# Optimization experiments

Hardware: AMD Instinct MI355X
Metric: run time of the kernel (lower is better)

## Reference

```python
import jax, jax.numpy as jnp
import numpy as np

B, T, H, V, ADIM, AMAX = 16, 1024, 512, 32000, 512, 10


def setup_inputs() -> dict:
    key = jax.random.key(0)
    ks = jax.random.split(key, 24)
    def n(k, shape, s=0.05):
        return jax.random.normal(k, shape, jnp.float32) * s
    return {
        "instruction": jax.random.randint(ks[0], (B, T), 0, V, dtype=jnp.int32),
        "emb": n(ks[1], (V, H)),
        "wih_f": n(ks[2], (4 * H, H)), "whh_f": n(ks[3], (4 * H, H)),
        "bih_f": n(ks[4], (4 * H,)), "bhh_f": n(ks[5], (4 * H,)),
        "wih_b": n(ks[6], (4 * H, H)), "whh_b": n(ks[7], (4 * H, H)),
        "bih_b": n(ks[8], (4 * H,)), "bhh_b": n(ks[9], (4 * H,)),
        "wg": n(ks[10], (2 * H, 2 * H)), "bg": n(ks[11], (2 * H,)),
        "ws1": n(ks[12], (H, 2 * H)), "bs1": n(ks[13], (H,)),
        "ws2": n(ks[14], (1, H)), "bs2": n(ks[15], (1,)),
        "wd1": n(ks[16], (H, 2 * H)), "bd1": n(ks[17], (H,)),
        "wd2": n(ks[18], (ADIM, H)), "bd2": n(ks[19], (ADIM,)),
        "max_actions": AMAX,
    }


def _lstm(x, wih, whh, bias):
    # x: [B, T, H] -> outputs [B, T, H]; PyTorch gate order i, f, g, o
    h0 = jnp.zeros((x.shape[0], whh.shape[1]), x.dtype)
    def step(carry, xt):
        h, c = carry
        g = xt @ wih.T + h @ whh.T + bias
        i, f, gg, o = jnp.split(g, 4, axis=-1)
        c = jax.nn.sigmoid(f) * c + jax.nn.sigmoid(i) * jnp.tanh(gg)
        h = jax.nn.sigmoid(o) * jnp.tanh(c)
        return (h, c), h
    _, hs = jax.lax.scan(step, (h0, h0), jnp.swapaxes(x, 0, 1))
    return jnp.swapaxes(hs, 0, 1)


def reference(instruction, emb, wih_f, whh_f, bih_f, bhh_f, wih_b, whh_b, bih_b, bhh_b,
              wg, bg, ws1, bs1, ws2, bs2, wd1, bd1, wd2, bd2, max_actions):
    x = emb[instruction]                                   # [B, T, H]
    fwd = _lstm(x, wih_f, whh_f, bih_f + bhh_f)            # [B, T, H]
    bwd = _lstm(x[:, ::-1], wih_b, whh_b, bih_b + bhh_b)[:, ::-1]
    enc = jnp.concatenate([fwd, bwd], axis=-1)             # [B, T, 2H]
    # sequence_lengths=None: h_n[0]=fwd last step, h_n[1]=bwd at t=0
    pooled = jnp.concatenate([fwd[:, -1], bwd[:, 0]], axis=-1)
    gctx = pooled @ wg.T + bg                               # [B, 2H]
    sh = jax.nn.relu(enc @ ws1.T + bs1)
    seg_probs = jax.nn.sigmoid((sh @ ws2.T + bs2)[..., 0])  # [B, T]
    mask = seg_probs > 0.5
    count = mask.sum(axis=-1)
    # first max_actions True positions per row (stable sort keeps time order)
    order = jnp.argsort(jnp.logical_not(mask), axis=1, stable=True)[:, :max_actions]
    gathered = jnp.take_along_axis(enc, order[..., None], axis=1)  # [B, A, 2H]
    slots = jnp.arange(max_actions)
    valid = slots[None, :] < jnp.minimum(count, max_actions)[:, None]
    empty = ((count == 0)[:, None]) & (slots[None, :] == 0)  # fallback: decode global ctx
    dec_in = jnp.where(valid[..., None], gathered, 0.0)
    dec_in = jnp.where(empty[..., None], gctx[:, None, :], dec_in)
    dh = jax.nn.relu(dec_in @ wd1.T + bd1)
    actions = (dh @ wd2.T + bd2) * (valid | empty)[..., None].astype(dec_in.dtype)
    return actions, seg_probs
```

## Files before the change

### kernel.cpp

```cpp
#include <hip/hip_runtime.h>
#include <math.h>

#define T   1024
#define NB  16
#define HD  512

#define OFF_BAR  0
#define OFF_HH   256
#define OFF_SH   (OFF_HH + 16777216)
#define OFF_SEGP (OFF_SH + 8388608)
#define OFF_GCTX (OFF_SEGP + 16384)
#define OFF_SEL  (OFF_GCTX + 16384)

typedef unsigned long long u64;

__device__ __forceinline__ float sigmoidf_(float x){ return 1.0f/(1.0f + __expf(-x)); }
__device__ __forceinline__ float tanhf_(float x){ return 1.0f - 2.0f/(1.0f + __expf(2.0f*x)); }

__global__ __launch_bounds__(512, 1)
void lstm_kernel(const int* __restrict__ instr, const float* __restrict__ emb,
                 const float* __restrict__ wih_f, const float* __restrict__ whh_f,
                 const float* __restrict__ bih_f, const float* __restrict__ bhh_f,
                 const float* __restrict__ wih_b, const float* __restrict__ whh_b,
                 const float* __restrict__ bih_b, const float* __restrict__ bhh_b,
                 float* __restrict__ ws)
{
    float* h_hist = ws + OFF_HH;

    const int wg     = blockIdx.x;
    const int dir    = wg & 1;
    const int bgrp   = (wg >> 1) & 3;
    const int uslice = wg >> 3;
    const int U      = uslice * 16;
    const int b0     = bgrp * 4;

    const float* wih = dir ? wih_b : wih_f;
    const float* whh = dir ? whh_b : whh_f;
    const float* bih = dir ? bih_b : bih_f;
    const float* bhh = dir ? bhh_b : bhh_f;

    const int tid  = threadIdx.x;
    const int wid  = tid >> 6;
    const int lane = tid & 63;
    const int rg   = wid;

    float wi[64], wh[64];
#pragma unroll
    for (int ri = 0; ri < 8; ++ri){
        int rgl = rg*8 + ri;
        int gate = rgl >> 4, ul = rgl & 15;
        size_t row = (size_t)(gate*HD + U + ul) * HD + lane*8;
        float4 a0 = *(const float4*)(wih + row);
        float4 a1 = *(const float4*)(wih + row + 4);
        float4 b0v = *(const float4*)(whh + row);
        float4 b1v = *(const float4*)(whh + row + 4);
        wi[ri*8+0]=a0.x; wi[ri*8+1]=a0.y; wi[ri*8+2]=a0.z; wi[ri*8+3]=a0.w;
        wi[ri*8+4]=a1.x; wi[ri*8+5]=a1.y; wi[ri*8+6]=a1.z; wi[ri*8+7]=a1.w;
        wh[ri*8+0]=b0v.x; wh[ri*8+1]=b0v.y; wh[ri*8+2]=b0v.z; wh[ri*8+3]=b0v.w;
        wh[ri*8+4]=b1v.x; wh[ri*8+5]=b1v.y; wh[ri*8+6]=b1v.z; wh[ri*8+7]=b1v.w;
    }

    float bI, bF, bG, bO, cst = 0.0f;
    {
        int u = tid & 15;
        bI = bih[0*HD + U + u] + bhh[0*HD + U + u];
        bF = bih[1*HD + U + u] + bhh[1*HD + U + u];
        bG = bih[2*HD + U + u] + bhh[2*HD + U + u];
        bO = bih[3*HD + U + u] + bhh[3*HD + U + u];
    }

    __shared__ float hxch[8*4*64];
    __shared__ float gbuf[256];

    const int jown = ((lane&1)<<4)|((lane&2)<<2)|(lane&4)|((lane&8)>>2)|((lane&16)>>4);
    const int own_bi  = jown >> 3;
    const int own_rgl = rg*8 + (jown & 7);
    const int gslot   = (own_rgl >> 4)*64 + own_bi*16 + (own_rgl & 15);

    for (int s = 0; s < T; ++s){
        const int tp = dir ? (T-1-s) : s;

        float a[32];
#pragma unroll
        for (int j = 0; j < 32; ++j) a[j] = 0.0f;

#pragma unroll
        for (int bi = 0; bi < 4; ++bi){
            int b = b0 + bi;
            int idx = instr[b*T + tp];
            const float* px = emb + (size_t)idx*HD + lane*8;
            float4 x0 = *(const float4*)px;
            float4 x1 = *(const float4*)(px + 4);
            float xs[8] = {x0.x,x0.y,x0.z,x0.w,x1.x,x1.y,x1.z,x1.w};
#pragma unroll
            for (int kk = 0; kk < 8; ++kk){
                float xv = xs[kk];
#pragma unroll
                for (int ri = 0; ri < 8; ++ri)
                    a[bi*8+ri] = fmaf(xv, wi[ri*8+kk], a[bi*8+ri]);
            }
        }

        if (s > 0){
            const int tprev = dir ? (T - s) : (s - 1);
            const float* hbase = h_hist + (size_t)(dir*T + tprev)*NB*HD;

            if (wid == 0){
                u64 pq[16];
                for (;;){
#pragma unroll
                    for (int bi = 0; bi < 4; ++bi){
                        const u64* p = (const u64*)(hbase + (size_t)(b0+bi)*HD + lane*8);
#pragma unroll
                        for (int q = 0; q < 4; ++q)
                            pq[bi*4+q] = __hip_atomic_load(p + q, __ATOMIC_RELAXED, __HIP_MEMORY_SCOPE_AGENT);
                    }
                    unsigned ok = 1u;
#pragma unroll
                    for (int j = 0; j < 16; ++j){
                        ok &= ((unsigned)(pq[j]      ) != 0xFFFFFFFFu) ? 1u : 0u;
                        ok &= ((unsigned)(pq[j] >> 32) != 0xFFFFFFFFu) ? 1u : 0u;
                    }
                    if (__all(ok != 0u)) break;
                    __builtin_amdgcn_s_sleep(1);
                }
#pragma unroll
                for (int bi = 0; bi < 4; ++bi){
#pragma unroll
                    for (int q = 0; q < 4; ++q){
                        hxch[(2*q  )*256 + bi*64 + lane] = __uint_as_float((unsigned)(pq[bi*4+q]      ));
                        hxch[(2*q+1)*256 + bi*64 + lane] = __uint_as_float((unsigned)(pq[bi*4+q] >> 32));
                    }
                }
            }
            __syncthreads();

#pragma unroll
            for (int bi = 0; bi < 4; ++bi){
                float hs[8];
#pragma unroll
                for (int kk = 0; kk < 8; ++kk)
                    hs[kk] = hxch[kk*256 + bi*64 + lane];
#pragma unroll
                for (int kk = 0; kk < 8; ++kk){
                    float hv = hs[kk];
#pragma unroll
                    for (int ri = 0; ri < 8; ++ri)
                        a[bi*8+ri] = fmaf(hv, wh[ri*8+kk], a[bi*8+ri]);
                }
            }
        }

#pragma unroll
        for (int m = 0; m < 5; ++m){
            const int half = 16 >> m;
            const bool up = (lane >> m) & 1;
#pragma unroll
            for (int j = 0; j < 16; ++j){
                if (j < half){
                    float lo = a[j], hi = a[j+half];
                    float rlo = __shfl_xor(lo, 1<<m, 64);
                    float rhi = __shfl_xor(hi, 1<<m, 64);
                    a[j] = up ? (hi + rhi) : (lo + rlo);
                }
            }
        }
        a[0] += __shfl_xor(a[0], 32, 64);

        if ((lane & 32) == 0) gbuf[gslot] = a[0];
        __syncthreads();

        if (tid < 64){
            float iv = sigmoidf_(gbuf[      tid] + bI);
            float fv = sigmoidf_(gbuf[ 64 + tid] + bF);
            float gv = tanhf_  (gbuf[128 + tid] + bG);
            float ov = sigmoidf_(gbuf[192 + tid] + bO);
            cst = fv*cst + iv*gv;
            float hv = ov * tanhf_(cst);
            int b = b0 + (tid >> 4), u = tid & 15;
            __hip_atomic_store(&h_hist[((size_t)(dir*T + tp)*NB + b)*HD + U + u], hv,
                               __ATOMIC_RELAXED, __HIP_MEMORY_SCOPE_AGENT);
        }
    }
}

__global__ __launch_bounds__(256, 2)
void seg_gemm(const float* __restrict__ ws_, const float* __restrict__ ws1,
              const float* __restrict__ bs1)
{
    const float* h_hist = ws_ + OFF_HH;
    float* SH = (float*)(ws_ + OFF_SH);
    __shared__ float As[64][17];
    __shared__ float Bs[64][17];
    const int m0 = blockIdx.x * 64;
    const int n0 = blockIdx.y * 64;
    const int tid = threadIdx.x;
    const int r  = tid >> 2;
    const int kq = (tid & 3) * 4;
    const int ty = tid >> 4, tx = tid & 15;
    const int bI = m0 >> 10;
    const int t0 = m0 & 1023;

    float acc[4][4];
#pragma unroll
    for (int i=0;i<4;i++)
#pragma unroll
        for (int j=0;j<4;j++) acc[i][j]=0.0f;

    for (int kb = 0; kb < 1024; kb += 16){
        int kk = kb + kq;
        const float* ap = (kk < 512)
            ? h_hist + ((size_t)(t0 + r)*NB + bI)*HD + kk
            : h_hist + ((size_t)(T + t0 + r)*NB + bI)*HD + (kk - 512);
        float4 av = *(const float4*)ap;
        As[r][kq+0]=av.x; As[r][kq+1]=av.y; As[r][kq+2]=av.z; As[r][kq+3]=av.w;
        float4 bv = *(const float4*)(ws1 + (size_t)(n0 + r)*1024 + kk);
        Bs[r][kq+0]=bv.x; Bs[r][kq+1]=bv.y; Bs[r][kq+2]=bv.z; Bs[r][kq+3]=bv.w;
        __syncthreads();
#pragma unroll
        for (int k2 = 0; k2 < 16; ++k2){
            float av_[4], bv_[4];
#pragma unroll
            for (int i=0;i<4;i++) av_[i] = As[ty*4+i][k2];
#pragma unroll
            for (int j=0;j<4;j++) bv_[j] = Bs[tx*4+j][k2];
#pragma unroll
            for (int i=0;i<4;i++)
#pragma unroll
                for (int j=0;j<4;j++) acc[i][j] = fmaf(av_[i], bv_[j], acc[i][j]);
        }
        __syncthreads();
    }
#pragma unroll
    for (int i=0;i<4;i++){
        int m = m0 + ty*4 + i;
#pragma unroll
        for (int j=0;j<4;j++){
            int n = n0 + tx*4 + j;
            SH[(size_t)m*512 + n] = fmaxf(acc[i][j] + bs1[n], 0.0f);
        }
    }
}

__global__ void seg_score(const float* __restrict__ ws_, const float* __restrict__ ws2,
                          const float* __restrict__ bs2, float* __restrict__ dout)
{
    const float* SH = ws_ + OFF_SH;
    float* segp = (float*)(ws_ + OFF_SEGP);
    int row  = blockIdx.x*4 + (threadIdx.x >> 6);
    int lane = threadIdx.x & 63;
    const float* p = SH + (size_t)row*512 + lane*8;
    const float* q = ws2 + lane*8;
    float4 a0=*(const float4*)p, a1=*(const float4*)(p+4);
    float4 b0=*(const float4*)q, b1=*(const float4*)(q+4);
    float ssum = a0.x*b0.x + a0.y*b0.y + a0.z*b0.z + a0.w*b0.w
               + a1.x*b1.x + a1.y*b1.y + a1.z*b1.z + a1.w*b1.w;
#pragma unroll
    for (int m=1;m<64;m<<=1) ssum += __shfl_xor(ssum, m, 64);
    if (lane == 0){
        float z = ssum + bs2[0];
        float pr = 1.0f/(1.0f + __expf(-z));
        segp[row] = pr;
        dout[81920 + row] = pr;
    }
}

__global__ void select_gctx(float* __restrict__ ws_, const float* __restrict__ wgm,
                            const float* __restrict__ bgv)
{
    const float* h_hist = ws_ + OFF_HH;
    const float* segp   = ws_ + OFF_SEGP;
    float* gctx = ws_ + OFF_GCTX;
    int* sel = (int*)(ws_ + OFF_SEL);
    int b = blockIdx.x, tid = threadIdx.x;
    __shared__ unsigned char flag[1024];
    __shared__ float pool[1024];
    for (int j = tid; j < 1024; j += 256){
        flag[j] = segp[b*1024 + j] > 0.5f ? 1 : 0;
        pool[j] = (j < 512) ? h_hist[((size_t)1023*NB + b)*HD + j]
                            : h_hist[((size_t)T*NB + b)*HD + (j - 512)];
    }
    __syncthreads();
    if (tid == 0){
        int c = 0;
        int tmp[10];
        for (int j = 0; j < 10; ++j) tmp[j] = 0;
        for (int t = 0; t < 1024; ++t){
            if (flag[t]){ if (c < 10) tmp[c] = t; c++; }
        }
        for (int j = 0; j < 10; ++j) sel[b*12 + j] = tmp[j];
        sel[b*12 + 10] = c;
        sel[b*12 + 11] = 0;
    }
    __syncthreads();
    for (int n = tid; n < 1024; n += 256){
        float acc = bgv[n];
        const float* wr = wgm + (size_t)n*1024;
        for (int k = 0; k < 1024; k += 4){
            acc += wr[k]*pool[k] + wr[k+1]*pool[k+1] + wr[k+2]*pool[k+2] + wr[k+3]*pool[k+3];
        }
        gctx[b*1024 + n] = acc;
    }
}

__global__ void decode(const float* __restrict__ ws_, const float* __restrict__ wd1,
                       const float* __restrict__ bd1, const float* __restrict__ wd2,
                       const float* __restrict__ bd2, float* __restrict__ dout)
{
    const float* h_hist = ws_ + OFF_HH;
    const float* gctx   = ws_ + OFF_GCTX;
    const int* sel = (const int*)(ws_ + OFF_SEL);
    int blk = blockIdx.x;
    int b = blk / 10, slot = blk % 10;
    int tid = threadIdx.x;
    int count = sel[b*12 + 10];
    int nval = count < 10 ? count : 10;
    bool empty = (count == 0);
    float* outp = dout + (size_t)(b*10 + slot)*512;
    if (slot >= nval && !(empty && slot == 0)){
        for (int n = tid; n < 512; n += 256) outp[n] = 0.0f;
        return;
    }
    __shared__ float row[1024];
    __shared__ float dh[512];
    if (empty){
        for (int j = tid; j < 1024; j += 256) row[j] = gctx[b*1024 + j];
    } else {
        int t = sel[b*12 + slot];
        for (int j = tid; j < 1024; j += 256)
            row[j] = (j < 512) ? h_hist[((size_t)t*NB + b)*HD + j]
                               : h_hist[((size_t)(T + t)*NB + b)*HD + (j-512)];
    }
    __syncthreads();
    for (int d = tid; d < 512; d += 256){
        float acc = bd1[d];
        const float* wr = wd1 + (size_t)d*1024;
        for (int k = 0; k < 1024; ++k) acc += wr[k]*row[k];
        dh[d] = fmaxf(acc, 0.0f);
    }
    __syncthreads();
    for (int n = tid; n < 512; n += 256){
        float acc = bd2[n];
        const float* wr = wd2 + (size_t)n*512;
        for (int k = 0; k < 512; ++k) acc += wr[k]*dh[k];
        outp[n] = acc;
    }
}

extern "C" void kernel_launch(void* const* d_in, const int* in_sizes, int n_in,
                              void* d_out, int out_size, void* d_ws, size_t ws_size,
                              hipStream_t stream)
{
    const int*   instr = (const int*)d_in[0];
    const float* emb   = (const float*)d_in[1];
    const float* wih_f = (const float*)d_in[2];
    const float* whh_f = (const float*)d_in[3];
    const float* bih_f = (const float*)d_in[4];
    const float* bhh_f = (const float*)d_in[5];
    const float* wih_b = (const float*)d_in[6];
    const float* whh_b = (const float*)d_in[7];
    const float* bih_b = (const float*)d_in[8];
    const float* bhh_b = (const float*)d_in[9];
    const float* wg_   = (const float*)d_in[10];
    const float* bg_   = (const float*)d_in[11];
    const float* ws1   = (const float*)d_in[12];
    const float* bs1   = (const float*)d_in[13];
    const float* ws2   = (const float*)d_in[14];
    const float* bs2   = (const float*)d_in[15];
    const float* wd1   = (const float*)d_in[16];
    const float* bd1   = (const float*)d_in[17];
    const float* wd2   = (const float*)d_in[18];
    const float* bd2   = (const float*)d_in[19];
    float* out = (float*)d_out;
    float* ws  = (float*)d_ws;

    hipMemsetAsync((char*)d_ws + (size_t)OFF_HH*4, 0xFF, (size_t)16777216*4, stream);

    hipLaunchKernelGGL(lstm_kernel, dim3(256), dim3(512), 0, stream,
                       instr, emb, wih_f, whh_f, bih_f, bhh_f,
                       wih_b, whh_b, bih_b, bhh_b, ws);
    hipLaunchKernelGGL(seg_gemm, dim3(256, 8), dim3(256), 0, stream, ws, ws1, bs1);
    hipLaunchKernelGGL(seg_score, dim3(4096), dim3(256), 0, stream, ws, ws2, bs2, out);
    hipLaunchKernelGGL(select_gctx, dim3(16), dim3(256), 0, stream, ws, wg_, bg_);
    hipLaunchKernelGGL(decode, dim3(160), dim3(256), 0, stream, ws, wd1, bd1, wd2, bd2, out);
}
```

Before: 4.390 ms.

## Poll per-group step counters before loading recurrent hidden state

Adds per-(direction, batch-group) flag arrays that each workgroup bumps after finishing a step. Waiters spin on a small 32-int flag vector instead of repeatedly atomically reloading the full hidden-state slice and checking for sentinel values. After the flags pass, the hidden state is read with plain vector loads, and the old sentinel check stays as a fallback re-read. The flag store is relaxed and not ordered after the other threads' h stores, so the sentinel check is still needed for correctness; it adds an extra flag store per step.

```diff
diff --git a/kernel.cpp b/kernel.cpp
--- a/kernel.cpp
+++ b/kernel.cpp
@@ -16,6 +16,18 @@
 
 __device__ __forceinline__ float sigmoidf_(float x){ return 1.0f/(1.0f + __expf(-x)); }
 __device__ __forceinline__ float tanhf_(float x){ return 1.0f - 2.0f/(1.0f + __expf(2.0f*x)); }
+
+__device__ __forceinline__ bool clean8(const float4* hq){
+    unsigned ok = 1u;
+#pragma unroll
+    for (int q = 0; q < 8; ++q){
+        ok &= (__float_as_uint(hq[q].x) != 0xFFFFFFFFu) ? 1u : 0u;
+        ok &= (__float_as_uint(hq[q].y) != 0xFFFFFFFFu) ? 1u : 0u;
+        ok &= (__float_as_uint(hq[q].z) != 0xFFFFFFFFu) ? 1u : 0u;
+        ok &= (__float_as_uint(hq[q].w) != 0xFFFFFFFFu) ? 1u : 0u;
+    }
+    return ok != 0u;
+}
 
 __global__ __launch_bounds__(512, 1)
 void lstm_kernel(const int* __restrict__ instr, const float* __restrict__ emb,
@@ -26,6 +38,7 @@
                  float* __restrict__ ws)
 {
     float* h_hist = ws + OFF_HH;
+    int* flags = (int*)ws;
 
     const int wg     = blockIdx.x;
     const int dir    = wg & 1;
@@ -33,6 +46,8 @@
     const int uslice = wg >> 3;
     const int U      = uslice * 16;
     const int b0     = bgrp * 4;
+
+    int* barf = flags + (dir*4 + bgrp)*32;
 
     const float* wih = dir ? wih_b : wih_f;
     const float* whh = dir ? whh_b : whh_f;
@@ -106,31 +121,46 @@
             const float* hbase = h_hist + (size_t)(dir*T + tprev)*NB*HD;
 
             if (wid == 0){
-                u64 pq[16];
                 for (;;){
+                    int v = (lane < 32)
+                        ? __hip_atomic_load(barf + lane, __ATOMIC_RELAXED, __HIP_MEMORY_SCOPE_AGENT)
+                        : 0x7fffffff;
+                    if (__all(v >= s)) break;
+                    __builtin_amdgcn_s_sleep(1);
+                }
+                float4 hq[8];
+#pragma unroll
+                for (int bi = 0; bi < 4; ++bi){
+                    const float* ph = hbase + (size_t)(b0+bi)*HD + lane*8;
+                    hq[bi*2]   = *(const float4*)ph;
+                    hq[bi*2+1] = *(const float4*)(ph + 4);
+                }
+                while (!__all(clean8(hq))){
 #pragma unroll
                     for (int bi = 0; bi < 4; ++bi){
                         const u64* p = (const u64*)(hbase + (size_t)(b0+bi)*HD + lane*8);
-#pragma unroll
-                        for (int q = 0; q < 4; ++q)
-                            pq[bi*4+q] = __hip_atomic_load(p + q, __ATOMIC_RELAXED, __HIP_MEMORY_SCOPE_AGENT);
+                        u64 q0 = __hip_atomic_load(p+0, __ATOMIC_RELAXED, __HIP_MEMORY_SCOPE_AGENT);
+                        u64 q1 = __hip_atomic_load(p+1, __ATOMIC_RELAXED, __HIP_MEMORY_SCOPE_AGENT);
+                        u64 q2 = __hip_atomic_load(p+2, __ATOMIC_RELAXED, __HIP_MEMORY_SCOPE_AGENT);
+                        u64 q3 = __hip_atomic_load(p+3, __ATOMIC_RELAXED, __HIP_MEMORY_SCOPE_AGENT);
+                        float2 f0 = __builtin_bit_cast(float2, q0);
+                        float2 f1 = __builtin_bit_cast(float2, q1);
+                        float2 f2 = __builtin_bit_cast(float2, q2);
+                        float2 f3 = __builtin_bit_cast(float2, q3);
+                        hq[bi*2]   = make_float4(f0.x, f0.y, f1.x, f1.y);
+                        hq[bi*2+1] = make_float4(f2.x, f2.y, f3.x, f3.y);
                     }
-                    unsigned ok = 1u;
-#pragma unroll
-                    for (int j = 0; j < 16; ++j){
-                        ok &= ((unsigned)(pq[j]      ) != 0xFFFFFFFFu) ? 1u : 0u;
-                        ok &= ((unsigned)(pq[j] >> 32) != 0xFFFFFFFFu) ? 1u : 0u;
-                    }
-                    if (__all(ok != 0u)) break;
-                    __builtin_amdgcn_s_sleep(1);
                 }
 #pragma unroll
                 for (int bi = 0; bi < 4; ++bi){
-#pragma unroll
-                    for (int q = 0; q < 4; ++q){
-                        hxch[(2*q  )*256 + bi*64 + lane] = __uint_as_float((unsigned)(pq[bi*4+q]      ));
-                        hxch[(2*q+1)*256 + bi*64 + lane] = __uint_as_float((unsigned)(pq[bi*4+q] >> 32));
-                    }
+                    hxch[0*256 + bi*64 + lane] = hq[bi*2].x;
+                    hxch[1*256 + bi*64 + lane] = hq[bi*2].y;
+                    hxch[2*256 + bi*64 + lane] = hq[bi*2].z;
+                    hxch[3*256 + bi*64 + lane] = hq[bi*2].w;
+                    hxch[4*256 + bi*64 + lane] = hq[bi*2+1].x;
+                    hxch[5*256 + bi*64 + lane] = hq[bi*2+1].y;
+                    hxch[6*256 + bi*64 + lane] = hq[bi*2+1].z;
+                    hxch[7*256 + bi*64 + lane] = hq[bi*2+1].w;
                 }
             }
             __syncthreads();
@@ -181,6 +211,8 @@
             __hip_atomic_store(&h_hist[((size_t)(dir*T + tp)*NB + b)*HD + U + u], hv,
                                __ATOMIC_RELAXED, __HIP_MEMORY_SCOPE_AGENT);
         }
+        if (tid == 0)
+            __hip_atomic_store(barf + uslice, s + 1, __ATOMIC_RELAXED, __HIP_MEMORY_SCOPE_AGENT);
     }
 }
 
@@ -374,6 +406,7 @@
     float* out = (float*)d_out;
     float* ws  = (float*)d_ws;
 
+    hipMemsetAsync(d_ws, 0, 1024, stream);
     hipMemsetAsync((char*)d_ws + (size_t)OFF_HH*4, 0xFF, (size_t)16777216*4, stream);
 
     hipLaunchKernelGGL(lstm_kernel, dim3(256), dim3(512), 0, stream,
```

After: 4.728 ms. 1.08x slower.
